# Kernel tuning notes

Measured on AMD Instinct MI355X. Metric: run time of the kernel, lower is better.

The kernel has to match this reference:

```python
import jax, jax.numpy as jnp
import numpy as np

HIDDEN = 768
HEADS = 12
HEAD_DIM = HIDDEN // HEADS  # 64


def setup_inputs() -> dict:
    key = jax.random.key(0)
    ks = jax.random.split(key, 8)
    B, S = 2, 2048
    hidden_states = jax.random.normal(ks[0], (B, S, HIDDEN), dtype=jnp.float32)
    attention_mask = jnp.zeros((B, 1, 1, S), dtype=jnp.float32)
    scale = 1.0 / np.sqrt(HIDDEN)
    Wq = jax.random.normal(ks[1], (HIDDEN, HIDDEN), dtype=jnp.float32) * scale
    bq = jnp.zeros((HIDDEN,), dtype=jnp.float32)
    Wk = jax.random.normal(ks[2], (HIDDEN, HIDDEN), dtype=jnp.float32) * scale
    bk = jnp.zeros((HIDDEN,), dtype=jnp.float32)
    Wv = jax.random.normal(ks[3], (HIDDEN, HIDDEN), dtype=jnp.float32) * scale
    bv = jnp.zeros((HIDDEN,), dtype=jnp.float32)
    return {
        "hidden_states": hidden_states,
        "attention_mask": attention_mask,
        "Wq": Wq, "bq": bq, "Wk": Wk, "bk": bk, "Wv": Wv, "bv": bv,
    }


def _split_heads(x):
    # [B, S, hidden] -> [B, H, S, D]
    B, S, _ = x.shape
    return x.reshape(B, S, HEADS, HEAD_DIM).transpose(0, 2, 1, 3)


def reference(hidden_states, attention_mask, Wq, bq, Wk, bk, Wv, bv):
    q = _split_heads(hidden_states @ Wq + bq)  # [B,H,S,D]
    k = _split_heads(hidden_states @ Wk + bk)
    v = _split_heads(hidden_states @ Wv + bv)
    scores = jnp.einsum('bhqd,bhkd->bhqk', q, k) / np.sqrt(HEAD_DIM)
    scores = scores + attention_mask  # broadcast [B,1,1,S]
    probs = jax.nn.softmax(scores, axis=-1)
    ctx = jnp.einsum('bhqk,bhkd->bhqd', probs, v)  # [B,H,S,D]
    B, H, S, D = ctx.shape
    return ctx.transpose(0, 2, 1, 3).reshape(B, S, H * D)
```

## Files before the change

kernel.cpp:

```cpp
#include <hip/hip_runtime.h>

#define HID 768
#define NHEAD 12
#define HD 64
#define SEQ 2048
#define BATCH 2
#define PH (BATCH * NHEAD * SEQ * HD)
#define XEL (BATCH * SEQ * HID)
#define LOG2E 1.4426950408889634f
#define C1 (0.125f * LOG2E)

typedef __attribute__((ext_vector_type(8))) short bf16x8;
typedef __attribute__((ext_vector_type(4))) short bf16x4;
typedef __attribute__((ext_vector_type(4))) float f32x4;
typedef __attribute__((ext_vector_type(16))) float f32x16;

static __device__ __forceinline__ short f2b(float f) {
  unsigned int u = __builtin_bit_cast(unsigned int, f);
  unsigned int r = (u + 0x7fffu + ((u >> 16) & 1u)) >> 16;
  return (short)(unsigned short)r;
}

static __device__ __forceinline__ float fexp2(float x) {
  float r; asm("v_exp_f32 %0, %1" : "=v"(r) : "v"(x)); return r;
}

__global__ __launch_bounds__(256) void prep(
    const float* __restrict__ X,
    const float* __restrict__ Wq, const float* __restrict__ Wk,
    const float* __restrict__ Wv, const float* __restrict__ mask,
    short* __restrict__ Xb, short* __restrict__ Wt, float* __restrict__ mask2)
{
  __shared__ short T[64][65];
  const int t = threadIdx.x;
  const int blk = blockIdx.x;
  if (blk < 768) {
    const size_t base = (size_t)blk * 4096 + t * 16;
    f32x4 a0 = *(const f32x4*)(X + base);
    f32x4 a1 = *(const f32x4*)(X + base + 4);
    f32x4 a2 = *(const f32x4*)(X + base + 8);
    f32x4 a3 = *(const f32x4*)(X + base + 12);
    bf16x8 o0, o1;
#pragma unroll
    for (int i = 0; i < 4; ++i) {
      o0[i] = f2b(a0[i]); o0[4 + i] = f2b(a1[i]);
      o1[i] = f2b(a2[i]); o1[4 + i] = f2b(a3[i]);
    }
    *(bf16x8*)(Xb + base) = o0;
    *(bf16x8*)(Xb + base + 8) = o1;
  } else if (blk < 1200) {
    const int wb   = blk - 768;
    const int mat  = wb / 144;
    const int tile = wb - mat * 144;
    const int r0 = (tile / 12) * 64;
    const int c0 = (tile % 12) * 64;
    const float* __restrict__ W = (mat == 0) ? Wq : (mat == 1 ? Wk : Wv);
#pragma unroll
    for (int i = 0; i < 4; ++i) {
      const int r = (t >> 4) + 16 * i;
      const int c = (t & 15) * 4;
      f32x4 v = *(const f32x4*)(W + (size_t)(r0 + r) * HID + c0 + c);
      T[r][c + 0] = f2b(v[0]); T[r][c + 1] = f2b(v[1]);
      T[r][c + 2] = f2b(v[2]); T[r][c + 3] = f2b(v[3]);
    }
    __syncthreads();
    const int cr = t >> 2;
    const int ck = (t & 3) * 16;
    bf16x8 u0, u1;
#pragma unroll
    for (int j = 0; j < 8; ++j) { u0[j] = T[ck + j][cr]; u1[j] = T[ck + 8 + j][cr]; }
    short* orow = Wt + (size_t)(mat * HID + c0 + cr) * HID + r0 + ck;
    *(bf16x8*)orow = u0;
    *(bf16x8*)(orow + 8) = u1;
  } else {
#pragma unroll
    for (int i = 0; i < 4; ++i) {
      const int idx = (t * 4 + i * 1024);
      f32x4 v = *(const f32x4*)(mask + idx);
      v *= LOG2E;
      *(f32x4*)(mask2 + idx) = v;
    }
  }
}

__global__ __launch_bounds__(256, 3) void qkv_gemm(
    const short* __restrict__ Xb, const short* __restrict__ Wt,
    const float* __restrict__ bq, const float* __restrict__ bk,
    const float* __restrict__ bv,
    short* __restrict__ Qb, short* __restrict__ Kb, short* __restrict__ Vt)
{
  __shared__ __align__(16) short SM[128 * 132];
  short (*A_lds)[64] = (short(*)[64])SM;
  short (*B_lds)[64] = (short(*)[64])(SM + 128 * 64);
  short (*Tv)[132]   = (short(*)[132])SM;

  const int tid = threadIdx.x;
  const int w  = tid >> 6;
  const int l  = tid & 63;
  const int lr = l & 15;
  const int g  = l >> 4;
  const int wm = w >> 1;
  const int wn = w & 1;

  const int raw = blockIdx.x;
  const int swz = (raw & 7) * 72 + (raw >> 3);
  const int by  = swz / 18;
  const int bx  = swz - by * 18;
  const int mb0 = by * 128;
  const int nb0 = bx * 128;

  const int lrow8 = l >> 3;
  const int lslot = (l & 7) ^ lrow8;
  const short* __restrict__ pA = Xb + (size_t)(mb0 + w * 32 + lrow8) * HID + lslot * 8;
  const short* __restrict__ pB = Wt + (size_t)(nb0 + w * 32 + lrow8) * HID + lslot * 8;

  f32x4 acc[4][4];
#pragma unroll
  for (int mi = 0; mi < 4; ++mi)
#pragma unroll
    for (int ni = 0; ni < 4; ++ni) acc[mi][ni] = (f32x4){0.f, 0.f, 0.f, 0.f};

  const int rsw = (lr & 7) << 3;

  for (int ks = 0; ks < HID / 64; ++ks) {
    const int k0 = ks * 64;
    __syncthreads();
#pragma unroll
    for (int i = 0; i < 4; ++i) {
      __builtin_amdgcn_global_load_lds(
          (const void*)(pA + k0 + i * 8 * HID), (void*)&A_lds[w * 32 + i * 8][0], 16, 0, 0);
      __builtin_amdgcn_global_load_lds(
          (const void*)(pB + k0 + i * 8 * HID), (void*)&B_lds[w * 32 + i * 8][0], 16, 0, 0);
    }
    __syncthreads();

#pragma unroll
    for (int h = 0; h < 2; ++h) {
      bf16x8 a[4], b[4];
#pragma unroll
      for (int i = 0; i < 4; ++i) {
        const int coff = (((h << 2) | g) << 3) ^ rsw;
        a[i] = *(const bf16x8*)&A_lds[wm * 64 + 16 * i + lr][coff];
        b[i] = *(const bf16x8*)&B_lds[wn * 64 + 16 * i + lr][coff];
      }
#pragma unroll
      for (int mi = 0; mi < 4; ++mi)
#pragma unroll
        for (int ni = 0; ni < 4; ++ni)
          acc[mi][ni] = __builtin_amdgcn_mfma_f32_16x16x32_bf16(a[mi], b[ni], acc[mi][ni], 0, 0, 0);
    }
  }

  const int mat  = nb0 / HID;
  const int n0   = nb0 + wn * 64;
  const int m0   = mb0 + wm * 64;
  const int colb = n0 - mat * HID;

  if (mat < 2) {
    const float* __restrict__ bias = (mat == 0) ? bq : bk;
    short* __restrict__ Out        = (mat == 0) ? Qb : Kb;
#pragma unroll
    for (int ni = 0; ni < 4; ++ni) {
      const int col = colb + 16 * ni + lr;
      const int h = col >> 6, d = col & 63;
      const float bias_v = bias[col];
#pragma unroll
      for (int mi = 0; mi < 4; ++mi) {
        const int mbase = m0 + 16 * mi + 4 * g;
#pragma unroll
        for (int r = 0; r < 4; ++r) {
          const int m = mbase + r;
          const int bb = m >> 11;
          const int s  = m & (SEQ - 1);
          Out[((size_t)(bb * NHEAD + h) * SEQ + s) * HD + d] = f2b(acc[mi][ni][r] + bias_v);
        }
      }
    }
  } else {
    __syncthreads();
#pragma unroll
    for (int ni = 0; ni < 4; ++ni) {
      const int col = colb + 16 * ni + lr;
      const float bias_v = bv[col];
      const int rowl = wn * 64 + 16 * ni + lr;
#pragma unroll
      for (int mi = 0; mi < 4; ++mi) {
        bf16x4 pk;
#pragma unroll
        for (int r = 0; r < 4; ++r) pk[r] = f2b(acc[mi][ni][r] + bias_v);
        *(bf16x4*)&Tv[rowl][wm * 64 + 16 * mi + 4 * g] = pk;
      }
    }
    __syncthreads();
    const int row  = tid >> 1;
    const int half = tid & 1;
    const int col  = nb0 - 2 * HID + row;
    const int h = col >> 6, d = col & 63;
    const int bb = mb0 >> 11;
    const int s0 = (mb0 & (SEQ - 1)) + half * 64;
    short* op = Vt + ((size_t)(bb * NHEAD + h) * HD + d) * SEQ + s0;
#pragma unroll
    for (int j = 0; j < 8; ++j)
      *(bf16x8*)(op + 8 * j) = *(const bf16x8*)&Tv[row][half * 64 + 8 * j];
  }
}

__global__ __launch_bounds__(256, 3) void attn_fwd(
    const short* __restrict__ Qb, const short* __restrict__ Kb,
    const short* __restrict__ Vt, const float* __restrict__ mask2,
    float* __restrict__ out)
{
  __shared__ __align__(16) short KA[2][64][64];
  __shared__ __align__(16) short VA[2][64][64];
  __shared__ __align__(16) short PA[4][32][72];

  const int tid  = threadIdx.x;
  const int w    = tid >> 6;
  const int pair = w >> 1;
  const int pw   = w & 1;
  const int l    = tid & 63;
  const int r5   = l & 31;
  const int hi   = l >> 5;

  const int bid  = blockIdx.x;
  const int xcd  = bid & 7;
  const int slot = bid >> 3;
  const int bh   = xcd * 3 + (slot >> 5);
  const int qblk = slot & 31;

  const int b    = bh / 12;
  const int hh   = bh - b * 12;
  const int q0   = qblk * 64 + pw * 32;
  const int kb   = pair * 1024;

  const short* __restrict__ Qh  = Qb + (size_t)bh * SEQ * HD;
  const short* __restrict__ Kh  = Kb + (size_t)bh * SEQ * HD;
  const short* __restrict__ Vth = Vt + (size_t)bh * HD * SEQ;
  const float* __restrict__ mb2 = mask2 + (size_t)b * SEQ;

  bf16x8 qf[4];
#pragma unroll
  for (int j = 0; j < 4; ++j)
    qf[j] = *(const bf16x8*)(Qh + (size_t)(q0 + r5) * HD + 16 * j + 8 * hi);

  f32x16 o0 = (f32x16){0.f};
  f32x16 o1 = (f32x16){0.f};
  float mrun = -INFINITY;
  float l_run = 0.f;

  const int ptid = tid & 127;
  const int sr = ptid >> 1;
  const int sb = (ptid & 1) * 4;
  const short* __restrict__ Kp = Kh + (size_t)(kb + sr) * HD + sb * 8;
  const short* __restrict__ Vp = Vth + (size_t)sr * SEQ + kb + sb * 8;
  const int ssw = sr & 7;

  bf16x8 kst[4], vst[4];
#pragma unroll
  for (int j = 0; j < 4; ++j) {
    kst[j] = *(const bf16x8*)(Kp + 8 * j);
    vst[j] = *(const bf16x8*)(Vp + 8 * j);
  }
#pragma unroll
  for (int j = 0; j < 4; ++j) {
    *(bf16x8*)&KA[pair][sr][((sb + j) ^ ssw) * 8] = kst[j];
    *(bf16x8*)&VA[pair][sr][((sb + j) ^ ssw) * 8] = vst[j];
  }

  const int rsw = r5 & 7;

  for (int t = 0; t < 16; ++t) {
    const int kv0 = kb + t * 64;
    __syncthreads();

    const size_t kvn = (size_t)(((t + 1) & 15) * 64);
#pragma unroll
    for (int j = 0; j < 4; ++j) {
      kst[j] = *(const bf16x8*)(Kp + kvn * HD + 8 * j);
      vst[j] = *(const bf16x8*)(Vp + kvn + 8 * j);
    }

    f32x16 st0 = (f32x16){0.f};
    f32x16 st1 = (f32x16){0.f};
    __builtin_amdgcn_s_setprio(1);
#pragma unroll
    for (int j = 0; j < 4; ++j) {
      const int co = ((2 * j + hi) ^ rsw) * 8;
      bf16x8 ka0 = *(const bf16x8*)&KA[pair][r5][co];
      bf16x8 ka1 = *(const bf16x8*)&KA[pair][32 + r5][co];
      st0 = __builtin_amdgcn_mfma_f32_32x32x16_bf16(ka0, qf[j], st0, 0, 0, 0);
      st1 = __builtin_amdgcn_mfma_f32_32x32x16_bf16(ka1, qf[j], st1, 0, 0, 0);
    }
    __builtin_amdgcn_s_setprio(0);

    float p[2][16];
#pragma unroll
    for (int t2 = 0; t2 < 4; ++t2) {
      f32x4 mv0 = *(const f32x4*)&mb2[kv0 + 8 * t2 + 4 * hi];
      f32x4 mv1 = *(const f32x4*)&mb2[kv0 + 32 + 8 * t2 + 4 * hi];
#pragma unroll
      for (int e = 0; e < 4; ++e) {
        p[0][4 * t2 + e] = st0[4 * t2 + e] * C1 + mv0[e];
        p[1][4 * t2 + e] = st1[4 * t2 + e] * C1 + mv1[e];
      }
    }
    float mx[8];
#pragma unroll
    for (int i = 0; i < 8; ++i)
      mx[i] = fmaxf(fmaxf(p[0][2 * i], p[0][2 * i + 1]),
                    fmaxf(p[1][2 * i], p[1][2 * i + 1]));
    float tm = fmaxf(fmaxf(fmaxf(mx[0], mx[1]), fmaxf(mx[2], mx[3])),
                     fmaxf(fmaxf(mx[4], mx[5]), fmaxf(mx[6], mx[7])));
    tm = fmaxf(tm, __shfl_xor(tm, 32, 64));

    if (__any(tm > mrun + 8.f)) {
      const float mn = fmaxf(mrun, tm);
      const float alpha = fexp2(mrun - mn);
      o0 *= alpha;
      o1 *= alpha;
      l_run *= alpha;
      mrun = mn;
    }

#pragma unroll
    for (int s2 = 0; s2 < 2; ++s2)
#pragma unroll
      for (int i = 0; i < 16; ++i) p[s2][i] = fexp2(p[s2][i] - mrun);
    float sm[8];
#pragma unroll
    for (int i = 0; i < 8; ++i)
      sm[i] = (p[0][2 * i] + p[0][2 * i + 1]) + (p[1][2 * i] + p[1][2 * i + 1]);
    float ts = ((sm[0] + sm[1]) + (sm[2] + sm[3])) + ((sm[4] + sm[5]) + (sm[6] + sm[7]));
    ts += __shfl_xor(ts, 32, 64);
    l_run += ts;

#pragma unroll
    for (int s2 = 0; s2 < 2; ++s2)
#pragma unroll
      for (int t2 = 0; t2 < 4; ++t2) {
        unsigned int u0, u1;
        asm("v_cvt_pk_bf16_f32 %0, %1, %2"
            : "=v"(u0) : "v"(p[s2][4 * t2 + 0]), "v"(p[s2][4 * t2 + 1]));
        asm("v_cvt_pk_bf16_f32 %0, %1, %2"
            : "=v"(u1) : "v"(p[s2][4 * t2 + 2]), "v"(p[s2][4 * t2 + 3]));
        uint2 uv; uv.x = u0; uv.y = u1;
        *(uint2*)&PA[w][r5][32 * s2 + 8 * t2 + 4 * hi] = uv;
      }

    bf16x8 pf[4];
#pragma unroll
    for (int j = 0; j < 4; ++j)
      pf[j] = *(const bf16x8*)&PA[w][r5][16 * j + 8 * hi];

    __builtin_amdgcn_s_setprio(1);
#pragma unroll
    for (int j = 0; j < 4; ++j) {
      const int co = ((2 * j + hi) ^ rsw) * 8;
      bf16x8 va0 = *(const bf16x8*)&VA[pair][r5][co];
      bf16x8 va1 = *(const bf16x8*)&VA[pair][32 + r5][co];
      o0 = __builtin_amdgcn_mfma_f32_32x32x16_bf16(va0, pf[j], o0, 0, 0, 0);
      o1 = __builtin_amdgcn_mfma_f32_32x32x16_bf16(va1, pf[j], o1, 0, 0, 0);
    }
    __builtin_amdgcn_s_setprio(0);

    __syncthreads();
#pragma unroll
    for (int j = 0; j < 4; ++j) {
      *(bf16x8*)&KA[pair][sr][((sb + j) ^ ssw) * 8] = kst[j];
      *(bf16x8*)&VA[pair][sr][((sb + j) ^ ssw) * 8] = vst[j];
    }
  }

  __syncthreads();
  float* Os = (float*)&KA[0][0][0];
  float* ML = (float*)&PA[0][0][0];

  if (w >= 2) {
    const int wv = w - 2;
    float* Or = Os + (size_t)(wv * 32 + r5) * 64;
#pragma unroll
    for (int t2 = 0; t2 < 4; ++t2) {
      f32x4 v0, v1;
#pragma unroll
      for (int e = 0; e < 4; ++e) { v0[e] = o0[4 * t2 + e]; v1[e] = o1[4 * t2 + e]; }
      *(f32x4*)&Or[8 * t2 + 4 * hi]      = v0;
      *(f32x4*)&Or[32 + 8 * t2 + 4 * hi] = v1;
    }
    if (hi == 0) {
      ML[wv * 64 + r5]      = mrun;
      ML[wv * 64 + 32 + r5] = l_run;
    }
  }
  __syncthreads();
  if (w < 2) {
    const float mo = ML[w * 64 + r5];
    const float lo = ML[w * 64 + 32 + r5];
    const float mm = fmaxf(mrun, mo);
    const float a0 = fexp2(mrun - mm);
    const float a1 = fexp2(mo - mm);
    const float inv = 1.f / (a0 * l_run + a1 * lo);
    const float* Or = Os + (size_t)(w * 32 + r5) * 64;
    float* ob = out + (size_t)(b * SEQ + q0 + r5) * HID + hh * HD;
#pragma unroll
    for (int t2 = 0; t2 < 4; ++t2) {
      f32x4 po = *(const f32x4*)&Or[8 * t2 + 4 * hi];
      f32x4 p1 = *(const f32x4*)&Or[32 + 8 * t2 + 4 * hi];
      f32x4 v0, v1;
#pragma unroll
      for (int e = 0; e < 4; ++e) {
        v0[e] = (a0 * o0[4 * t2 + e] + a1 * po[e]) * inv;
        v1[e] = (a0 * o1[4 * t2 + e] + a1 * p1[e]) * inv;
      }
      *(f32x4*)&ob[8 * t2 + 4 * hi]      = v0;
      *(f32x4*)&ob[32 + 8 * t2 + 4 * hi] = v1;
    }
  }
}

extern "C" void kernel_launch(void* const* d_in, const int* in_sizes, int n_in,
                              void* d_out, int out_size, void* d_ws, size_t ws_size,
                              hipStream_t stream) {
  const float* X    = (const float*)d_in[0];
  const float* mask = (const float*)d_in[1];
  const float* Wq   = (const float*)d_in[2];
  const float* bq   = (const float*)d_in[3];
  const float* Wk   = (const float*)d_in[4];
  const float* bk   = (const float*)d_in[5];
  const float* Wv   = (const float*)d_in[6];
  const float* bv   = (const float*)d_in[7];
  float* out = (float*)d_out;

  short* Qb = (short*)d_ws;
  short* Kb = Qb + PH;
  short* Vt = Kb + PH;
  short* Xb = Vt + PH;
  short* Wt = Xb + XEL;
  float* mask2 = (float*)(Wt + (size_t)3 * HID * HID);

  prep<<<dim3(1201), 256, 0, stream>>>(X, Wq, Wk, Wv, mask, Xb, Wt, mask2);
  qkv_gemm<<<dim3(576), 256, 0, stream>>>(Xb, Wt, bq, bk, bv, Qb, Kb, Vt);
  attn_fwd<<<dim3(768), 256, 0, stream>>>(Qb, Kb, Vt, mask2, out);
}
```

Before: 90.31 us.

## Load K/V MFMA fragments directly from global memory instead of LDS staging

Removes the LDS staging buffers for K and V, along with the per-iteration barriers and the register prefetch of the next tile. Each wave now loads its own K and V MFMA operand fragments straight from global memory, relying on L1/L2 to serve the copy shared by the two waves of a pair. The V loads are issued before the softmax so their latency can overlap with it. The epilogue scratch space is moved into the P buffer. This cuts LDS traffic, synchronisation and LDS footprint, but K loads sit right before the MFMAs with no prefetch, and each pair fetches the same K/V twice from cache.

```diff
diff --git a/kernel.cpp b/kernel.cpp
--- a/kernel.cpp
+++ b/kernel.cpp
@@ -210,8 +210,6 @@
     const short* __restrict__ Vt, const float* __restrict__ mask2,
     float* __restrict__ out)
 {
-  __shared__ __align__(16) short KA[2][64][64];
-  __shared__ __align__(16) short VA[2][64][64];
   __shared__ __align__(16) short PA[4][32][72];
 
   const int tid  = threadIdx.x;
@@ -248,36 +246,21 @@
   float mrun = -INFINITY;
   float l_run = 0.f;
 
-  const int ptid = tid & 127;
-  const int sr = ptid >> 1;
-  const int sb = (ptid & 1) * 4;
-  const short* __restrict__ Kp = Kh + (size_t)(kb + sr) * HD + sb * 8;
-  const short* __restrict__ Vp = Vth + (size_t)sr * SEQ + kb + sb * 8;
-  const int ssw = sr & 7;
-
-  bf16x8 kst[4], vst[4];
-#pragma unroll
-  for (int j = 0; j < 4; ++j) {
-    kst[j] = *(const bf16x8*)(Kp + 8 * j);
-    vst[j] = *(const bf16x8*)(Vp + 8 * j);
-  }
-#pragma unroll
-  for (int j = 0; j < 4; ++j) {
-    *(bf16x8*)&KA[pair][sr][((sb + j) ^ ssw) * 8] = kst[j];
-    *(bf16x8*)&VA[pair][sr][((sb + j) ^ ssw) * 8] = vst[j];
-  }
-
-  const int rsw = r5 & 7;
+  const short* __restrict__ Ka = Kh + (size_t)(kb + r5) * HD + 8 * hi;
+  const short* __restrict__ Kc = Kh + (size_t)(kb + 32 + r5) * HD + 8 * hi;
+  const short* __restrict__ Va = Vth + (size_t)r5 * SEQ + kb + 8 * hi;
+  const short* __restrict__ Vc = Vth + (size_t)(32 + r5) * SEQ + kb + 8 * hi;
 
   for (int t = 0; t < 16; ++t) {
     const int kv0 = kb + t * 64;
-    __syncthreads();
-
-    const size_t kvn = (size_t)(((t + 1) & 15) * 64);
+    const size_t ko = (size_t)(t * 64) * HD;
+    const int    vo = t * 64;
+
+    bf16x8 ka0[4], ka1[4];
 #pragma unroll
     for (int j = 0; j < 4; ++j) {
-      kst[j] = *(const bf16x8*)(Kp + kvn * HD + 8 * j);
-      vst[j] = *(const bf16x8*)(Vp + kvn + 8 * j);
+      ka0[j] = *(const bf16x8*)(Ka + ko + 16 * j);
+      ka1[j] = *(const bf16x8*)(Kc + ko + 16 * j);
     }
 
     f32x16 st0 = (f32x16){0.f};
@@ -285,13 +268,17 @@
     __builtin_amdgcn_s_setprio(1);
 #pragma unroll
     for (int j = 0; j < 4; ++j) {
-      const int co = ((2 * j + hi) ^ rsw) * 8;
-      bf16x8 ka0 = *(const bf16x8*)&KA[pair][r5][co];
-      bf16x8 ka1 = *(const bf16x8*)&KA[pair][32 + r5][co];
-      st0 = __builtin_amdgcn_mfma_f32_32x32x16_bf16(ka0, qf[j], st0, 0, 0, 0);
-      st1 = __builtin_amdgcn_mfma_f32_32x32x16_bf16(ka1, qf[j], st1, 0, 0, 0);
+      st0 = __builtin_amdgcn_mfma_f32_32x32x16_bf16(ka0[j], qf[j], st0, 0, 0, 0);
+      st1 = __builtin_amdgcn_mfma_f32_32x32x16_bf16(ka1[j], qf[j], st1, 0, 0, 0);
     }
     __builtin_amdgcn_s_setprio(0);
+
+    bf16x8 va0[4], va1[4];
+#pragma unroll
+    for (int j = 0; j < 4; ++j) {
+      va0[j] = *(const bf16x8*)(Va + vo + 16 * j);
+      va1[j] = *(const bf16x8*)(Vc + vo + 16 * j);
+    }
 
     float p[2][16];
 #pragma unroll
@@ -355,25 +342,15 @@
     __builtin_amdgcn_s_setprio(1);
 #pragma unroll
     for (int j = 0; j < 4; ++j) {
-      const int co = ((2 * j + hi) ^ rsw) * 8;
-      bf16x8 va0 = *(const bf16x8*)&VA[pair][r5][co];
-      bf16x8 va1 = *(const bf16x8*)&VA[pair][32 + r5][co];
-      o0 = __builtin_amdgcn_mfma_f32_32x32x16_bf16(va0, pf[j], o0, 0, 0, 0);
-      o1 = __builtin_amdgcn_mfma_f32_32x32x16_bf16(va1, pf[j], o1, 0, 0, 0);
+      o0 = __builtin_amdgcn_mfma_f32_32x32x16_bf16(va0[j], pf[j], o0, 0, 0, 0);
+      o1 = __builtin_amdgcn_mfma_f32_32x32x16_bf16(va1[j], pf[j], o1, 0, 0, 0);
     }
     __builtin_amdgcn_s_setprio(0);
-
-    __syncthreads();
-#pragma unroll
-    for (int j = 0; j < 4; ++j) {
-      *(bf16x8*)&KA[pair][sr][((sb + j) ^ ssw) * 8] = kst[j];
-      *(bf16x8*)&VA[pair][sr][((sb + j) ^ ssw) * 8] = vst[j];
-    }
   }
 
   __syncthreads();
-  float* Os = (float*)&KA[0][0][0];
-  float* ML = (float*)&PA[0][0][0];
+  float* Os = (float*)&PA[0][0][0];
+  float* ML = Os + 2 * 32 * 64;
 
   if (w >= 2) {
     const int wv = w - 2;
```

Result: slower. 132.0 us (+46.2%).
